# Kernel optimization log

Measured on AMD Instinct MI355X. Metric: run time of the kernel, lower is better.

The kernel has to match this reference:

```python
import jax, jax.numpy as jnp
import numpy as np

N_HEADS, D_MODEL, D_K, D_V = 16, 1024, 64, 64
B, S = 2, 2048

def setup_inputs() -> dict:
    key = jax.random.key(0)
    k = jax.random.split(key, 7)
    s = 1.0 / np.sqrt(D_MODEL)
    return {
        "input_Q": jax.random.normal(k[0], (B, S, D_MODEL), jnp.float32),
        "input_K": jax.random.normal(k[1], (B, S, D_MODEL), jnp.float32),
        "input_V": jax.random.normal(k[2], (B, S, D_MODEL), jnp.float32),
        "W_Q": jax.random.normal(k[3], (D_MODEL, N_HEADS * D_K), jnp.float32) * s,
        "W_K": jax.random.normal(k[4], (D_MODEL, N_HEADS * D_K), jnp.float32) * s,
        "W_V": jax.random.normal(k[5], (D_MODEL, N_HEADS * D_V), jnp.float32) * s,
        "W_O": jax.random.normal(k[6], (N_HEADS * D_V, D_MODEL), jnp.float32) * s,
    }

def reference(input_Q, input_K, input_V, W_Q, W_K, W_V, W_O):
    b = input_Q.shape[0]
    # project and split heads: [b, h, s, d]
    Q = (input_Q @ W_Q).reshape(b, -1, N_HEADS, D_K).transpose(0, 2, 1, 3)
    K = (input_K @ W_K).reshape(b, -1, N_HEADS, D_K).transpose(0, 2, 1, 3)
    V = (input_V @ W_V).reshape(b, -1, N_HEADS, D_V).transpose(0, 2, 1, 3)
    scores = jnp.einsum("bhqd,bhkd->bhqk", Q, K) / np.sqrt(D_K)
    attn = jax.nn.softmax(scores, axis=-1)
    context = jnp.einsum("bhqk,bhkd->bhqd", attn, V)
    context = context.transpose(0, 2, 1, 3).reshape(b, -1, N_HEADS * D_V)
    out = context @ W_O + input_Q  # residual
    # LayerNorm instantiated fresh in torch forward -> gamma=1, beta=0
    mu = jnp.mean(out, axis=-1, keepdims=True)
    var = jnp.var(out, axis=-1, keepdims=True)
    return (out - mu) / jnp.sqrt(var + 1e-5)
```

## Files before the change

### kernel.cpp

```cpp
#include <hip/hip_runtime.h>
#include <hip/hip_bf16.h>
#include <cstdint>
#include <cstddef>

#define DEVFN __device__ __forceinline__

typedef __attribute__((ext_vector_type(8))) short short8;
typedef __attribute__((ext_vector_type(4))) float f32x4;
typedef __attribute__((ext_vector_type(16))) float f32x16;
typedef __attribute__((ext_vector_type(4))) unsigned short us4;

static constexpr int S_LEN = 2048;
static constexpr int DM    = 1024;
static constexpr int H     = 16;
static constexpr int DK    = 64;
static constexpr int BATCH = 2;
static constexpr int MROWS = BATCH * S_LEN;

DEVFN unsigned short f2bf(float f) {
  union { float f; unsigned int u; } x; x.f = f;
  unsigned int r = x.u + 0x7fffu + ((x.u >> 16) & 1u);
  return (unsigned short)(r >> 16);
}

DEVFN float fast_exp2(float x) { return __builtin_amdgcn_exp2f(x); }

DEVFN f32x4 mfma16(short8 a, short8 b, f32x4 c) {
  return __builtin_amdgcn_mfma_f32_16x16x32_bf16(a, b, c, 0, 0, 0);
}

DEVFN f32x16 mfma32(short8 a, short8 b, f32x16 c) {
  return __builtin_amdgcn_mfma_f32_32x32x16_bf16(a, b, c, 0, 0, 0);
}

DEVFN unsigned int cvtpk(float lo, float hi) {
  unsigned int r;
  asm("v_cvt_pk_bf16_f32 %0, %1, %2" : "=v"(r) : "v"(lo), "v"(hi));
  return r;
}

DEVFN void gload_lds16(const void* g, void* l) {
  __builtin_amdgcn_global_load_lds(
      (const __attribute__((address_space(1))) void*)g,
      (__attribute__((address_space(3))) void*)l, 16, 0, 0);
}

__global__ __launch_bounds__(256) void wt_transpose(
    const float* __restrict__ Wq, const float* __restrict__ Wk,
    const float* __restrict__ Wv, const float* __restrict__ Wo,
    unsigned short* __restrict__ Tq, unsigned short* __restrict__ Tk,
    unsigned short* __restrict__ Tv, unsigned short* __restrict__ To)
{
  const float* W = blockIdx.z == 0 ? Wq : blockIdx.z == 1 ? Wk : blockIdx.z == 2 ? Wv : Wo;
  unsigned short* T = blockIdx.z == 0 ? Tq : blockIdx.z == 1 ? Tk : blockIdx.z == 2 ? Tv : To;
  __shared__ float tile[32][33];
  int n0 = blockIdx.x * 32, k0 = blockIdx.y * 32;
  int tx = threadIdx.x & 31, ty = threadIdx.x >> 5;
#pragma unroll
  for (int i = 0; i < 4; ++i)
    tile[ty + 8 * i][tx] = W[(size_t)(k0 + ty + 8 * i) * DM + n0 + tx];
  __syncthreads();
#pragma unroll
  for (int i = 0; i < 4; ++i) {
    int n = ty + 8 * i;
    T[(size_t)(n0 + n) * DM + k0 + tx] = f2bf(tile[tx][n]);
  }
}

__global__ __launch_bounds__(256) void gemm_qkv(
    const float* __restrict__ Xq, const float* __restrict__ Xk, const float* __restrict__ Xv,
    const unsigned short* __restrict__ Tq, const unsigned short* __restrict__ Tk,
    const unsigned short* __restrict__ Tv,
    unsigned short* __restrict__ Qb, unsigned short* __restrict__ Kb,
    unsigned short* __restrict__ Vt)
{
  __shared__ __align__(16) unsigned short As[2][128][40];
  __shared__ __align__(16) unsigned short Bs[2][128 * 32];

  const int z = blockIdx.z;
  const float* X = z == 0 ? Xq : z == 1 ? Xk : Xv;
  const unsigned short* T = z == 0 ? Tq : z == 1 ? Tk : Tv;

  const int tid = threadIdx.x;
  const int lane = tid & 63, w = tid >> 6;
  const int wm = w >> 1, wn = w & 1;
  const int lr = lane & 15, lg = lane >> 4;
  const int m0 = blockIdx.x * 128, n0 = blockIdx.y * 128;

  const int arow = tid >> 1;
  const int acol = (tid & 1) * 16;
  const float* Arow = X + (size_t)(m0 + arow) * DM + acol;

  const int brr = lane >> 2, bsc = lane & 3;

  float4 a4[4];
  auto loadA = [&](int k0) {
#pragma unroll
    for (int j = 0; j < 4; ++j) a4[j] = *(const float4*)(Arow + k0 + j * 4);
  };
  auto writeA = [&](int buf) {
#pragma unroll
    for (int j = 0; j < 4; ++j) {
      us4 u;
      u.x = f2bf(a4[j].x); u.y = f2bf(a4[j].y);
      u.z = f2bf(a4[j].z); u.w = f2bf(a4[j].w);
      *(us4*)&As[buf][arow][acol + j * 4] = u;
    }
  };
  auto stageB = [&](int buf, int k0) {
#pragma unroll
    for (int i = 0; i < 2; ++i) {
      const int rr = (w * 2 + i) * 16 + brr;
      const int sc = (bsc ^ ((rr >> 1) & 3)) * 8;
      gload_lds16(T + (size_t)(n0 + rr) * DM + k0 + sc, &Bs[buf][(w * 2 + i) * 512]);
    }
  };

  f32x4 acc[4][4];
#pragma unroll
  for (int m = 0; m < 4; ++m)
#pragma unroll
    for (int n = 0; n < 4; ++n) acc[m][n] = (f32x4){0.f, 0.f, 0.f, 0.f};

  loadA(0);
  stageB(0, 0);
  writeA(0);
  __syncthreads();

  int buf = 0;
  for (int kt = 0; kt < DM / 32; ++kt) {
    const bool more = (kt + 1) < DM / 32;
    if (more) { loadA((kt + 1) * 32); stageB(buf ^ 1, (kt + 1) * 32); }

    short8 af[4], bfr[4];
#pragma unroll
    for (int m = 0; m < 4; ++m)
      af[m] = *(const short8*)&As[buf][wm * 64 + m * 16 + lr][lg * 8];
#pragma unroll
    for (int n = 0; n < 4; ++n) {
      const int row = wn * 64 + n * 16 + lr;
      const int ch = lg ^ ((row >> 1) & 3);
      bfr[n] = *(const short8*)&Bs[buf][row * 32 + ch * 8];
    }
#pragma unroll
    for (int m = 0; m < 4; ++m)
#pragma unroll
      for (int n = 0; n < 4; ++n) acc[m][n] = mfma16(af[m], bfr[n], acc[m][n]);

    if (more) writeA(buf ^ 1);
    __syncthreads();
    buf ^= 1;
  }

  if (z < 2) {
    const float scale = (z == 0) ? 0.125f * 1.44269504088896f : 1.0f;
    unsigned short* out = z == 0 ? Qb : Kb;
#pragma unroll
    for (int m = 0; m < 4; ++m)
#pragma unroll
      for (int n = 0; n < 4; ++n) {
        int col = n0 + wn * 64 + n * 16 + lr;
        int h = col >> 6, d = col & 63;
#pragma unroll
        for (int r = 0; r < 4; ++r) {
          int row = m0 + wm * 64 + m * 16 + lg * 4 + r;
          int b = row >> 11, s = row & (S_LEN - 1);
          out[((size_t)(b * H + h) * S_LEN + s) * DK + d] = f2bf(acc[m][n][r] * scale);
        }
      }
  } else {
#pragma unroll
    for (int m = 0; m < 4; ++m)
#pragma unroll
      for (int n = 0; n < 4; ++n) {
        int col = n0 + wn * 64 + n * 16 + lr;
        int h = col >> 6, d = col & 63;
        int row = m0 + wm * 64 + m * 16 + lg * 4;
        int b = row >> 11, s = row & (S_LEN - 1);
        us4 u;
#pragma unroll
        for (int r = 0; r < 4; ++r) u[r] = f2bf(acc[m][n][r]);
        *(us4*)(Vt + ((size_t)(b * H + h) * DK + d) * S_LEN + s) = u;
      }
  }
}

__global__ __launch_bounds__(256, 2) void attn(
    const unsigned short* __restrict__ Qg, const unsigned short* __restrict__ Kg,
    const unsigned short* __restrict__ Vg, unsigned short* __restrict__ ctx)
{
  constexpr int KBLK = 64;
  constexpr int NT = S_LEN / KBLK;
  __shared__ __align__(16) unsigned short Ks[2][KBLK][DK];
  __shared__ __align__(16) unsigned short Vs[2][DK][KBLK];

  const int tid = threadIdx.x, lane = tid & 63, w = tid >> 6;
  const int l31 = lane & 31, hi = lane >> 5;

  const int orig = blockIdx.x;
  const int id = (orig & 7) * 64 + (orig >> 3);
  const int bh = id >> 4, qb = id & 15;
  const int b = bh >> 4, h = bh & 15;
  const int q = qb * 128 + w * 32 + l31;

  const unsigned short* Qbh = Qg + (size_t)bh * S_LEN * DK;
  const unsigned short* Kbh = Kg + (size_t)bh * S_LEN * DK;
  const unsigned short* Vbh = Vg + (size_t)bh * DK * S_LEN;

  const int srow = lane >> 3;
  const int sslot = ((lane & 7) ^ srow) * 8;

  auto stage = [&](int buf, int t) {
    const int kbase = t * KBLK;
#pragma unroll
    for (int c = 0; c < 2; ++c) {
      const int rbase = w * 8 + c * 32;
      gload_lds16(Kbh + (size_t)(kbase + rbase + srow) * DK + sslot, &Ks[buf][rbase][0]);
      gload_lds16(Vbh + (size_t)(rbase + srow) * S_LEN + kbase + sslot, &Vs[buf][rbase][0]);
    }
  };

  short8 qf[4];
#pragma unroll
  for (int kk = 0; kk < 4; ++kk)
    qf[kk] = *(const short8*)(Qbh + (size_t)q * DK + kk * 16 + hi * 8);

  f32x16 o0, o1;
#pragma unroll
  for (int i = 0; i < 16; ++i) { o0[i] = 0.f; o1[i] = 0.f; }
  float mrun = -1e30f, lrun = 0.f;

  const int swz = (l31 & 7) << 4;

  stage(0, 0);
  __syncthreads();

  int buf = 0;
  for (int t = 0; t < NT; ++t) {
    if (t + 1 < NT) stage(buf ^ 1, t + 1);

    const char* Kb = (const char*)&Ks[buf][0][0];
    const char* Vb = (const char*)&Vs[buf][0][0];

    f32x16 s0, s1;
#pragma unroll
    for (int i = 0; i < 16; ++i) { s0[i] = 0.f; s1[i] = 0.f; }
#pragma unroll
    for (int kk = 0; kk < 4; ++kk) {
      const int cb = (kk * 32 + hi * 16) ^ swz;
      short8 ka0 = *(const short8*)(Kb + l31 * 128 + cb);
      short8 ka1 = *(const short8*)(Kb + (32 + l31) * 128 + cb);
      s0 = mfma32(ka0, qf[kk], s0);
      s1 = mfma32(ka1, qf[kk], s1);
    }

    float a[16];
#pragma unroll
    for (int i = 0; i < 16; ++i) a[i] = fmaxf(s0[i], s1[i]);
#pragma unroll
    for (int st = 8; st >= 1; st >>= 1)
#pragma unroll
      for (int i = 0; i < st; ++i) a[i] = fmaxf(a[i], a[i + st]);
    const float mx = fmaxf(a[0], __shfl_xor(a[0], 32, 64));

    const float mnew = fmaxf(mrun, mx);
    const float alpha = fast_exp2(mrun - mnew);
    mrun = mnew;

#pragma unroll
    for (int i = 0; i < 16; ++i) {
      s0[i] = fast_exp2(s0[i] - mnew);
      s1[i] = fast_exp2(s1[i] - mnew);
    }

    float d0[16];
#pragma unroll
    for (int i = 0; i < 16; ++i) d0[i] = s0[i] + s1[i];
#pragma unroll
    for (int st = 8; st >= 1; st >>= 1)
#pragma unroll
      for (int i = 0; i < st; ++i) d0[i] = d0[i] + d0[i + st];
    const float ps = d0[0] + __shfl_xor(d0[0], 32, 64);
    lrun = lrun * alpha + ps;

#pragma unroll
    for (int i = 0; i < 16; ++i) { o0[i] *= alpha; o1[i] *= alpha; }

    short8 pf[4];
#pragma unroll
    for (int sl = 0; sl < 4; ++sl) {
      const f32x16& sv = (sl & 2) ? s1 : s0;
      const int base = (sl & 1) * 8;
      const unsigned int a01 = cvtpk(sv[base + 0], sv[base + 1]);
      const unsigned int a23 = cvtpk(sv[base + 2], sv[base + 3]);
      const unsigned int b01 = cvtpk(sv[base + 4], sv[base + 5]);
      const unsigned int b23 = cvtpk(sv[base + 6], sv[base + 7]);
      const unsigned int x0 = __shfl_xor(hi ? a01 : b01, 32, 64);
      const unsigned int x1 = __shfl_xor(hi ? a23 : b23, 32, 64);
      union { unsigned int u[4]; short8 v; } pu;
      pu.u[0] = hi ? x0 : a01;
      pu.u[1] = hi ? x1 : a23;
      pu.u[2] = hi ? b01 : x0;
      pu.u[3] = hi ? b23 : x1;
      pf[sl] = pu.v;
    }

#pragma unroll
    for (int sl = 0; sl < 4; ++sl) {
      const int cb = (sl * 32 + hi * 16) ^ swz;
      short8 va0 = *(const short8*)(Vb + l31 * 128 + cb);
      short8 va1 = *(const short8*)(Vb + (32 + l31) * 128 + cb);
      o0 = mfma32(va0, pf[sl], o0);
      o1 = mfma32(va1, pf[sl], o1);
    }

    __syncthreads();
    buf ^= 1;
  }

  const float rinv = 1.0f / lrun;
  unsigned short* crow = ctx + ((size_t)(b * S_LEN + q)) * DM + h * DK;
#pragma unroll
  for (int n = 0; n < 2; ++n) {
#pragma unroll
    for (int r = 0; r < 16; r += 2) {
      const float v0 = (n ? o1[r] : o0[r]) * rinv;
      const float v1 = (n ? o1[r + 1] : o0[r + 1]) * rinv;
      const int d = (r & 3) + 8 * (r >> 2) + 4 * hi + 32 * n;
      *(unsigned int*)(crow + d) = cvtpk(v0, v1);
    }
  }
}

__global__ __launch_bounds__(256, 3) void gemm_out(
    const unsigned short* __restrict__ C, const unsigned short* __restrict__ To,
    const float* __restrict__ resid, float* __restrict__ y)
{
  __shared__ __align__(16) unsigned short As[2][128 * 32];
  __shared__ __align__(16) unsigned short Bs[2][64 * 32];

  const int tid = threadIdx.x;
  const int lane = tid & 63, w = tid >> 6;
  const int wm = w >> 1, wn = w & 1;
  const int lr = lane & 15, lg = lane >> 4;
  const int m0 = blockIdx.x * 128, n0 = blockIdx.y * 64;

  const int brr = lane >> 2, bsc = lane & 3;

  auto stage = [&](int buf, int k0) {
#pragma unroll
    for (int i = 0; i < 2; ++i) {
      const int rr = (w * 2 + i) * 16 + brr;
      const int sc = (bsc ^ ((rr >> 1) & 3)) * 8;
      gload_lds16(C + (size_t)(m0 + rr) * DM + k0 + sc, &As[buf][(w * 2 + i) * 512]);
    }
    const int rr = w * 16 + brr;
    const int sc = (bsc ^ ((rr >> 1) & 3)) * 8;
    gload_lds16(To + (size_t)(n0 + rr) * DM + k0 + sc, &Bs[buf][w * 512]);
  };

  f32x4 acc[4][2];
#pragma unroll
  for (int m = 0; m < 4; ++m)
#pragma unroll
    for (int n = 0; n < 2; ++n) acc[m][n] = (f32x4){0.f, 0.f, 0.f, 0.f};

  stage(0, 0);
  __syncthreads();

  int buf = 0;
  for (int kt = 0; kt < DM / 32; ++kt) {
    if (kt + 1 < DM / 32) stage(buf ^ 1, (kt + 1) * 32);
    short8 af[4], bfr[2];
#pragma unroll
    for (int m = 0; m < 4; ++m) {
      const int row = wm * 64 + m * 16 + lr;
      const int ch = lg ^ ((row >> 1) & 3);
      af[m] = *(const short8*)&As[buf][row * 32 + ch * 8];
    }
#pragma unroll
    for (int n = 0; n < 2; ++n) {
      const int row = wn * 32 + n * 16 + lr;
      const int ch = lg ^ ((row >> 1) & 3);
      bfr[n] = *(const short8*)&Bs[buf][row * 32 + ch * 8];
    }
#pragma unroll
    for (int m = 0; m < 4; ++m)
#pragma unroll
      for (int n = 0; n < 2; ++n) acc[m][n] = mfma16(af[m], bfr[n], acc[m][n]);
    __syncthreads();
    buf ^= 1;
  }

#pragma unroll
  for (int m = 0; m < 4; ++m)
#pragma unroll
    for (int n = 0; n < 2; ++n) {
      int col = n0 + wn * 32 + n * 16 + lr;
#pragma unroll
      for (int r = 0; r < 4; ++r) {
        int row = m0 + wm * 64 + m * 16 + lg * 4 + r;
        size_t idx = (size_t)row * DM + col;
        y[idx] = acc[m][n][r] + resid[idx];
      }
    }
}

__global__ __launch_bounds__(256) void lnorm(const float* __restrict__ y, float* __restrict__ out)
{
  const int row = blockIdx.x;
  const int tid = threadIdx.x;
  const float4 v = ((const float4*)(y + (size_t)row * DM))[tid];
  float s = v.x + v.y + v.z + v.w;
  float sq = v.x * v.x + v.y * v.y + v.z * v.z + v.w * v.w;
  s += __shfl_xor(s, 1, 64);  sq += __shfl_xor(sq, 1, 64);
  s += __shfl_xor(s, 2, 64);  sq += __shfl_xor(sq, 2, 64);
  s += __shfl_xor(s, 4, 64);  sq += __shfl_xor(sq, 4, 64);
  s += __shfl_xor(s, 8, 64);  sq += __shfl_xor(sq, 8, 64);
  s += __shfl_xor(s, 16, 64); sq += __shfl_xor(sq, 16, 64);
  s += __shfl_xor(s, 32, 64); sq += __shfl_xor(sq, 32, 64);
  __shared__ float ps[4], pq[4];
  int w = tid >> 6, lane = tid & 63;
  if (lane == 0) { ps[w] = s; pq[w] = sq; }
  __syncthreads();
  s = ps[0] + ps[1] + ps[2] + ps[3];
  sq = pq[0] + pq[1] + pq[2] + pq[3];
  float mean = s * (1.0f / DM);
  float var = sq * (1.0f / DM) - mean * mean;
  float rstd = rsqrtf(var + 1e-5f);
  float4 ov;
  ov.x = (v.x - mean) * rstd;
  ov.y = (v.y - mean) * rstd;
  ov.z = (v.z - mean) * rstd;
  ov.w = (v.w - mean) * rstd;
  ((float4*)(out + (size_t)row * DM))[tid] = ov;
}

extern "C" void kernel_launch(void* const* d_in, const int* in_sizes, int n_in,
                              void* d_out, int out_size, void* d_ws, size_t ws_size,
                              hipStream_t stream) {
  const float* Xq = (const float*)d_in[0];
  const float* Xk = (const float*)d_in[1];
  const float* Xv = (const float*)d_in[2];
  const float* Wq = (const float*)d_in[3];
  const float* Wk = (const float*)d_in[4];
  const float* Wv = (const float*)d_in[5];
  const float* Wo = (const float*)d_in[6];
  float* out = (float*)d_out;
  char* ws = (char*)d_ws;

  const size_t WT_BYTES  = (size_t)DM * DM * 2;
  const size_t QKV_BYTES = (size_t)BATCH * H * S_LEN * DK * 2;
  const size_t CTX_BYTES = (size_t)MROWS * DM * 2;

  size_t off = 0;
  auto take = [&](size_t bytes) { size_t o = off; off += (bytes + 255) & ~(size_t)255; return o; };
  unsigned short* Tq  = (unsigned short*)(ws + take(WT_BYTES));
  unsigned short* Tk  = (unsigned short*)(ws + take(WT_BYTES));
  unsigned short* Tv  = (unsigned short*)(ws + take(WT_BYTES));
  unsigned short* To  = (unsigned short*)(ws + take(WT_BYTES));
  size_t qb_off = take(QKV_BYTES);
  unsigned short* Qb  = (unsigned short*)(ws + qb_off);
  unsigned short* Kb  = (unsigned short*)(ws + take(QKV_BYTES));
  unsigned short* Vt  = (unsigned short*)(ws + take(QKV_BYTES));
  unsigned short* Ctx = (unsigned short*)(ws + take(CTX_BYTES));
  float* y = (float*)(ws + qb_off);

  if (ws_size < off) return;

  wt_transpose<<<dim3(32, 32, 4), 256, 0, stream>>>(Wq, Wk, Wv, Wo, Tq, Tk, Tv, To);
  gemm_qkv<<<dim3(32, 8, 3), 256, 0, stream>>>(Xq, Xk, Xv, Tq, Tk, Tv, Qb, Kb, Vt);
  attn<<<dim3(512), 256, 0, stream>>>(Qb, Kb, Vt, Ctx);
  gemm_out<<<dim3(32, 16), 256, 0, stream>>>(Ctx, To, Xq, y);
  lnorm<<<MROWS, 256, 0, stream>>>(y, out);
}
```

Measured before the change: 146.1 us.

## Pre-convert QKV inputs to bf16 and stage both GEMM operands via direct LDS loads

```diff
diff --git a/kernel.cpp b/kernel.cpp
--- a/kernel.cpp
+++ b/kernel.cpp
@@ -67,18 +67,33 @@
   }
 }
 
-__global__ __launch_bounds__(256) void gemm_qkv(
-    const float* __restrict__ Xq, const float* __restrict__ Xk, const float* __restrict__ Xv,
+__global__ __launch_bounds__(256) void xcvt3(
+    const float* __restrict__ X0, const float* __restrict__ X1,
+    const float* __restrict__ X2, unsigned short* __restrict__ Y)
+{
+  const float* X = blockIdx.y == 0 ? X0 : blockIdx.y == 1 ? X1 : X2;
+  unsigned short* Yz = Y + (size_t)blockIdx.y * MROWS * DM;
+  const size_t i = ((size_t)blockIdx.x * 256 + threadIdx.x) * 8;
+  float4 v0 = *(const float4*)(X + i);
+  float4 v1 = *(const float4*)(X + i + 4);
+  union { us4 u[2]; short8 s; } r;
+  r.u[0].x = f2bf(v0.x); r.u[0].y = f2bf(v0.y); r.u[0].z = f2bf(v0.z); r.u[0].w = f2bf(v0.w);
+  r.u[1].x = f2bf(v1.x); r.u[1].y = f2bf(v1.y); r.u[1].z = f2bf(v1.z); r.u[1].w = f2bf(v1.w);
+  *(short8*)(Yz + i) = r.s;
+}
+
+__global__ __launch_bounds__(256, 3) void gemm_qkv(
+    const unsigned short* __restrict__ Xb,
     const unsigned short* __restrict__ Tq, const unsigned short* __restrict__ Tk,
     const unsigned short* __restrict__ Tv,
     unsigned short* __restrict__ Qb, unsigned short* __restrict__ Kb,
     unsigned short* __restrict__ Vt)
 {
-  __shared__ __align__(16) unsigned short As[2][128][40];
+  __shared__ __align__(16) unsigned short As[2][128 * 32];
   __shared__ __align__(16) unsigned short Bs[2][128 * 32];
 
   const int z = blockIdx.z;
-  const float* X = z == 0 ? Xq : z == 1 ? Xk : Xv;
+  const unsigned short* A = Xb + (size_t)z * MROWS * DM;
   const unsigned short* T = z == 0 ? Tq : z == 1 ? Tk : Tv;
 
   const int tid = threadIdx.x;
@@ -87,34 +102,17 @@
   const int lr = lane & 15, lg = lane >> 4;
   const int m0 = blockIdx.x * 128, n0 = blockIdx.y * 128;
 
-  const int arow = tid >> 1;
-  const int acol = (tid & 1) * 16;
-  const float* Arow = X + (size_t)(m0 + arow) * DM + acol;
-
-  const int brr = lane >> 2, bsc = lane & 3;
-
-  float4 a4[4];
-  auto loadA = [&](int k0) {
-#pragma unroll
-    for (int j = 0; j < 4; ++j) a4[j] = *(const float4*)(Arow + k0 + j * 4);
+  const int srw = lane >> 2, sch = lane & 3;
+
+  auto stage = [&](int buf, int k0) {
+#pragma unroll
+    for (int i = 0; i < 2; ++i) {
+      const int rr = (w * 2 + i) * 16 + srw;
+      const int sc = (sch ^ ((rr >> 1) & 3)) * 8;
+      gload_lds16(A + (size_t)(m0 + rr) * DM + k0 + sc, &As[buf][(w * 2 + i) * 512]);
+      gload_lds16(T + (size_t)(n0 + rr) * DM + k0 + sc, &Bs[buf][(w * 2 + i) * 512]);
+    }
   };
-  auto writeA = [&](int buf) {
-#pragma unroll
-    for (int j = 0; j < 4; ++j) {
-      us4 u;
-      u.x = f2bf(a4[j].x); u.y = f2bf(a4[j].y);
-      u.z = f2bf(a4[j].z); u.w = f2bf(a4[j].w);
-      *(us4*)&As[buf][arow][acol + j * 4] = u;
-    }
-  };
-  auto stageB = [&](int buf, int k0) {
-#pragma unroll
-    for (int i = 0; i < 2; ++i) {
-      const int rr = (w * 2 + i) * 16 + brr;
-      const int sc = (bsc ^ ((rr >> 1) & 3)) * 8;
-      gload_lds16(T + (size_t)(n0 + rr) * DM + k0 + sc, &Bs[buf][(w * 2 + i) * 512]);
-    }
-  };
 
   f32x4 acc[4][4];
 #pragma unroll
@@ -122,20 +120,19 @@
 #pragma unroll
     for (int n = 0; n < 4; ++n) acc[m][n] = (f32x4){0.f, 0.f, 0.f, 0.f};
 
-  loadA(0);
-  stageB(0, 0);
-  writeA(0);
+  stage(0, 0);
   __syncthreads();
 
   int buf = 0;
   for (int kt = 0; kt < DM / 32; ++kt) {
-    const bool more = (kt + 1) < DM / 32;
-    if (more) { loadA((kt + 1) * 32); stageB(buf ^ 1, (kt + 1) * 32); }
-
+    if (kt + 1 < DM / 32) stage(buf ^ 1, (kt + 1) * 32);
     short8 af[4], bfr[4];
 #pragma unroll
-    for (int m = 0; m < 4; ++m)
-      af[m] = *(const short8*)&As[buf][wm * 64 + m * 16 + lr][lg * 8];
+    for (int m = 0; m < 4; ++m) {
+      const int row = wm * 64 + m * 16 + lr;
+      const int ch = lg ^ ((row >> 1) & 3);
+      af[m] = *(const short8*)&As[buf][row * 32 + ch * 8];
+    }
 #pragma unroll
     for (int n = 0; n < 4; ++n) {
       const int row = wn * 64 + n * 16 + lr;
@@ -146,8 +143,6 @@
     for (int m = 0; m < 4; ++m)
 #pragma unroll
       for (int n = 0; n < 4; ++n) acc[m][n] = mfma16(af[m], bfr[n], acc[m][n]);
-
-    if (more) writeA(buf ^ 1);
     __syncthreads();
     buf ^= 1;
   }
@@ -450,8 +445,8 @@
   char* ws = (char*)d_ws;
 
   const size_t WT_BYTES  = (size_t)DM * DM * 2;
+  const size_t XB_BYTES  = (size_t)3 * MROWS * DM * 2;
   const size_t QKV_BYTES = (size_t)BATCH * H * S_LEN * DK * 2;
-  const size_t CTX_BYTES = (size_t)MROWS * DM * 2;
 
   size_t off = 0;
   auto take = [&](size_t bytes) { size_t o = off; off += (bytes + 255) & ~(size_t)255; return o; };
@@ -459,17 +454,19 @@
   unsigned short* Tk  = (unsigned short*)(ws + take(WT_BYTES));
   unsigned short* Tv  = (unsigned short*)(ws + take(WT_BYTES));
   unsigned short* To  = (unsigned short*)(ws + take(WT_BYTES));
-  size_t qb_off = take(QKV_BYTES);
-  unsigned short* Qb  = (unsigned short*)(ws + qb_off);
+  size_t xb_off = take(XB_BYTES);
+  unsigned short* Xb  = (unsigned short*)(ws + xb_off);
+  unsigned short* Qb  = (unsigned short*)(ws + take(QKV_BYTES));
   unsigned short* Kb  = (unsigned short*)(ws + take(QKV_BYTES));
   unsigned short* Vt  = (unsigned short*)(ws + take(QKV_BYTES));
-  unsigned short* Ctx = (unsigned short*)(ws + take(CTX_BYTES));
-  float* y = (float*)(ws + qb_off);
+  unsigned short* Ctx = Xb;
+  float* y = (float*)(ws + xb_off + (size_t)MROWS * DM * 2);
 
   if (ws_size < off) return;
 
   wt_transpose<<<dim3(32, 32, 4), 256, 0, stream>>>(Wq, Wk, Wv, Wo, Tq, Tk, Tv, To);
-  gemm_qkv<<<dim3(32, 8, 3), 256, 0, stream>>>(Xq, Xk, Xv, Tq, Tk, Tv, Qb, Kb, Vt);
+  xcvt3<<<dim3(2048, 3), 256, 0, stream>>>(Xq, Xk, Xv, Xb);
+  gemm_qkv<<<dim3(32, 8, 3), 256, 0, stream>>>(Xb, Tq, Tk, Tv, Qb, Kb, Vt);
   attn<<<dim3(512), 256, 0, stream>>>(Qb, Kb, Vt, Ctx);
   gemm_out<<<dim3(32, 16), 256, 0, stream>>>(Ctx, To, Xq, y);
   lnorm<<<MROWS, 256, 0, stream>>>(y, out);
```

Result: faster. 142.8 us (-2.2%).
